# Optimization experiments

Measured on AMD Instinct MI355X. Metric: run time of the kernel, lower is better.

Reference implementation:

```python
import jax, jax.numpy as jnp
import numpy as np

B, V, D, H, W = 2, 256, 512, 256, 256
CH = 96  # RED-CNN channels


def conv2d(x, w, b=None, padding='SAME'):
    y = jax.lax.conv_general_dilated(x, w, (1, 1), padding,
                                     dimension_numbers=('NCHW', 'OIHW', 'NCHW'))
    if b is not None:
        y = y + b[None, :, None, None]
    return y


def backproject_per_view(fp, angles):
    # fp: [B,V,D] filtered sinogram; one single-view backprojection per angle -> [B,V,H,W]
    b = fp.shape[0]
    ys = jnp.arange(H, dtype=jnp.float32) - (H - 1) / 2.
    xs = jnp.arange(W, dtype=jnp.float32) - (W - 1) / 2.
    Y, X = jnp.meshgrid(ys, xs, indexing='ij')
    c = jnp.cos(angles)[:, None, None]
    s = jnp.sin(angles)[:, None, None]
    u = X[None] * c + Y[None] * s + (D - 1) / 2.  # [V,H,W] detector coordinate
    u0 = jnp.floor(u)
    frac = (u - u0).reshape(1, V, H * W)
    u0i = u0.astype(jnp.int32)
    valid = ((u0i >= 0) & (u0i <= D - 2)).reshape(1, V, H * W)
    u0c = jnp.clip(u0i, 0, D - 2).reshape(V, H * W)
    idx0 = jnp.broadcast_to(u0c[None], (b, V, H * W))
    g0 = jnp.take_along_axis(fp, idx0, axis=2)
    g1 = jnp.take_along_axis(fp, idx0 + 1, axis=2)
    g = (g0 * (1. - frac) + g1 * frac) * valid
    return (g * (jnp.pi / V)).reshape(b, V, H, W)


def red_cnn(x, enc_w0, enc_w, enc_b, dec_w, dec_wN, dec_b, dec_bN):
    relu = jax.nn.relu
    r1 = x
    h = relu(conv2d(x, enc_w0, enc_b[0]))
    h = relu(conv2d(h, enc_w[0], enc_b[1])); r2 = h
    h = relu(conv2d(h, enc_w[1], enc_b[2]))
    h = relu(conv2d(h, enc_w[2], enc_b[3])); r3 = h
    h = relu(conv2d(h, enc_w[3], enc_b[4]))
    h = relu(conv2d(h, dec_w[0], dec_b[0]) + r3)
    h = relu(conv2d(h, dec_w[1], dec_b[1]))
    h = relu(conv2d(h, dec_w[2], dec_b[2]) + r2)
    h = relu(conv2d(h, dec_w[3], dec_b[3]))
    return relu(conv2d(h, dec_wN, dec_bN) + r1)


def setup_inputs():
    key = jax.random.key(0)
    ks = jax.random.split(key, 8)
    p = jax.random.normal(ks[0], (B, 1, V, D), dtype=jnp.float32)
    proj_weight = jax.random.uniform(ks[1], (1, 1, V, D), dtype=jnp.float32, minval=0.5, maxval=1.5)
    # Ram-Lak ramp filter, length 2*D-1 (matches padding=(0, num_det-1))
    n = np.arange(-(D - 1), D)
    h = np.zeros(2 * D - 1, dtype=np.float32)
    h[D - 1] = 0.25
    odd = (n % 2) != 0
    h[odd] = -1.0 / (np.pi * n[odd]) ** 2
    ramp = jnp.asarray(h).reshape(1, 1, 1, 2 * D - 1)
    views = jnp.arange(V, dtype=jnp.float32) * (2 * jnp.pi / V)
    std = 0.01
    conv_w = std * jax.random.normal(ks[2], (1, V, 3, 3), dtype=jnp.float32)
    conv_b = jnp.zeros((1,), jnp.float32)
    enc_w0 = std * jax.random.normal(ks[3], (CH, 1, 5, 5), dtype=jnp.float32)
    enc_w = std * jax.random.normal(ks[4], (4, CH, CH, 5, 5), dtype=jnp.float32)
    enc_b = jnp.zeros((5, CH), jnp.float32)
    dec_w = std * jax.random.normal(ks[5], (4, CH, CH, 5, 5), dtype=jnp.float32)
    dec_wN = std * jax.random.normal(ks[6], (1, CH, 5, 5), dtype=jnp.float32)
    dec_b = jnp.zeros((4, CH), jnp.float32)
    dec_bN = jnp.zeros((1,), jnp.float32)
    return dict(p=p, proj_weight=proj_weight, ramp=ramp, views=views,
                conv_w=conv_w, conv_b=conv_b, enc_w0=enc_w0, enc_w=enc_w,
                enc_b=enc_b, dec_w=dec_w, dec_wN=dec_wN, dec_b=dec_b, dec_bN=dec_bN)


def reference(p, proj_weight, ramp, views, conv_w, conv_b, enc_w0, enc_w,
              enc_b, dec_w, dec_wN, dec_b, dec_bN):
    p_w = p * proj_weight
    filtered = conv2d(p_w, ramp, padding=[(0, 0), (D - 1, D - 1)])  # [B,1,V,D]
    x = backproject_per_view(filtered[:, 0], views)                 # [B,V,H,W]
    x_sorted = jnp.sort(x, axis=1)                                  # cross-view sort
    x_in = conv2d(x_sorted, conv_w, conv_b)                         # [B,1,H,W]
    return red_cnn(x_in, enc_w0, enc_w, enc_b, dec_w, dec_wN, dec_b, dec_bN)
```

## Files before the change

kernel.cpp:

```cpp
#include <hip/hip_runtime.h>
#include <hip/hip_fp16.h>
#include <math.h>

#define B_ 2
#define V_ 256
#define D_ 512
#define H_ 256
#define W_ 256
#define CH_ 96

typedef _Float16 f16;
typedef f16 half8 __attribute__((ext_vector_type(8)));
typedef f16 half4 __attribute__((ext_vector_type(4)));
typedef f16 half2v __attribute__((ext_vector_type(2)));
typedef float f32x16 __attribute__((ext_vector_type(16)));

#if defined(__has_builtin)
#if __has_builtin(__builtin_amdgcn_fdot2)
#define FDOT2(a, b, c) __builtin_amdgcn_fdot2((a), (b), (c), false)
#endif
#endif
#ifndef FDOT2
#define FDOT2(a, b, c) ((c) + (float)(a)[0] * (float)(b)[0] + (float)(a)[1] * (float)(b)[1])
#endif


__global__ void filter_kernel(const float* __restrict__ p,
                              const float* __restrict__ pw,
                              const float* __restrict__ ramp,
                              float* __restrict__ filt) {
  int v = blockIdx.x, b = blockIdx.y, t = threadIdx.x;
  __shared__ float s_pw[D_];
  __shared__ float s_ramp[2 * D_ - 1];
  const float* prow = p + (size_t)(b * V_ + v) * D_;
  const float* wrow = pw + (size_t)v * D_;
  s_pw[t] = prow[t] * wrow[t];
  s_pw[t + 256] = prow[t + 256] * wrow[t + 256];
  for (int i = t; i < 2 * D_ - 1; i += 256) s_ramp[i] = ramp[i];
  __syncthreads();
  float acc0 = 0.f, acc1 = 0.f;
  for (int m = 0; m < D_; ++m) {
    float x = s_pw[m];
    acc0 += x * s_ramp[m - t + (D_ - 1)];
    acc1 += x * s_ramp[m - (t + 256) + (D_ - 1)];
  }
  filt[(size_t)(b * V_ + v) * D_ + t] = acc0;
  filt[(size_t)(b * V_ + v) * D_ + t + 256] = acc1;
}

__global__ __launch_bounds__(256) void backproj_sort_kernel(
    const float* __restrict__ filt,
    const float* __restrict__ views,
    f16* __restrict__ xt) {
  __shared__ float s_c[V_], s_s[V_];
  int tid = threadIdx.x;
  int b = blockIdx.y;
  {
    float sn, cs;
    sincosf(views[tid], &sn, &cs);
    s_c[tid] = cs;
    s_s[tid] = sn;
  }
  __syncthreads();
  int lane = tid & 63;
  int wv = tid >> 6;
  int pix = blockIdx.x * 4 + wv;
  int h = pix >> 8, w = pix & 255;
  float X = (float)w - (W_ - 1) * 0.5f;
  float Y = (float)h - (H_ - 1) * 0.5f;
  const float* filt_b = filt + (size_t)b * V_ * D_;
  float r[4];
  #pragma unroll
  for (int i = 0; i < 4; ++i) {
    int v = lane * 4 + i;
    float u = X * s_c[v] + Y * s_s[v] + (D_ - 1) * 0.5f;
    float u0 = floorf(u);
    float frac = u - u0;
    int u0i = (int)u0;
    bool valid = (u0i >= 0) && (u0i <= D_ - 2);
    int u0c = min(max(u0i, 0), D_ - 2);
    const float* frow = filt_b + (size_t)v * D_;
    float g0 = frow[u0c], g1 = frow[u0c + 1];
    r[i] = valid ? (g0 * (1.f - frac) + g1 * frac) * (float)(M_PI / V_) : 0.f;
  }
  half2v A = { (f16)r[0], (f16)r[1] };
  half2v B = { (f16)r[2], (f16)r[3] };
  #pragma unroll
  for (int k = 2; k <= 256; k <<= 1) {
    #pragma unroll
    for (int j = k >> 1; j > 0; j >>= 1) {
      if (j >= 4) {
        int jl = j >> 2;
        bool low = (lane & jl) == 0;
        bool up = (lane & (k >> 2)) == 0;
        bool keepmin = (low == up);
        int ia = __builtin_bit_cast(int, A);
        int ib = __builtin_bit_cast(int, B);
        half2v Ao = __builtin_bit_cast(half2v, __shfl_xor(ia, jl, 64));
        half2v Bo = __builtin_bit_cast(half2v, __shfl_xor(ib, jl, 64));
        half2v Amn = __builtin_elementwise_min(A, Ao);
        half2v Amx = __builtin_elementwise_max(A, Ao);
        half2v Bmn = __builtin_elementwise_min(B, Bo);
        half2v Bmx = __builtin_elementwise_max(B, Bo);
        A = keepmin ? Amn : Amx;
        B = keepmin ? Bmn : Bmx;
      } else if (j == 2) {
        bool up = (lane & (k >> 2)) == 0;
        half2v mn = __builtin_elementwise_min(A, B);
        half2v mx = __builtin_elementwise_max(A, B);
        A = up ? mn : mx;
        B = up ? mx : mn;
      } else {
        unsigned ua = __builtin_bit_cast(unsigned, A);
        unsigned ub = __builtin_bit_cast(unsigned, B);
        half2v As = __builtin_bit_cast(half2v, (ua >> 16) | (ua << 16));
        half2v Bs = __builtin_bit_cast(half2v, (ub >> 16) | (ub << 16));
        unsigned amn = __builtin_bit_cast(unsigned, __builtin_elementwise_min(A, As));
        unsigned amx = __builtin_bit_cast(unsigned, __builtin_elementwise_max(A, As));
        unsigned bmn = __builtin_bit_cast(unsigned, __builtin_elementwise_min(B, Bs));
        unsigned bmx = __builtin_bit_cast(unsigned, __builtin_elementwise_max(B, Bs));
        unsigned Aasc  = (amn & 0xFFFFu) | (amx & 0xFFFF0000u);
        unsigned Adesc = (amx & 0xFFFFu) | (amn & 0xFFFF0000u);
        unsigned Basc  = (bmn & 0xFFFFu) | (bmx & 0xFFFF0000u);
        unsigned Bdesc = (bmx & 0xFFFFu) | (bmn & 0xFFFF0000u);
        bool upA, upB;
        if (k == 2) { upA = true; upB = false; }
        else { upA = upB = ((lane & (k >> 2)) == 0); }
        A = __builtin_bit_cast(half2v, upA ? Aasc : Adesc);
        B = __builtin_bit_cast(half2v, upB ? Basc : Bdesc);
      }
    }
  }
  half4 o;
  o[0] = A[0]; o[1] = A[1]; o[2] = B[0]; o[3] = B[1];
  *(half4*)(xt + ((size_t)b * (H_ * W_) + pix) * V_ + lane * 4) = o;
}

__global__ __launch_bounds__(256) void conv_vred_kernel(
    const f16* __restrict__ xt,
    const float* __restrict__ cw,
    const float* __restrict__ cb,
    float* __restrict__ xin) {
  int tid = threadIdx.x;
  int b = blockIdx.y;
  int lane = tid & 63, wv = tid >> 6;
  int pix = blockIdx.x * 4 + wv;
  int h = pix >> 8, w = pix & 255;
  const f16* xtb = xt + (size_t)b * (H_ * W_) * V_;
  float wr[9][4];
  #pragma unroll
  for (int tap = 0; tap < 9; ++tap)
    #pragma unroll
    for (int i = 0; i < 4; ++i)
      wr[tap][i] = cw[(lane * 4 + i) * 9 + tap];
  float acc = 0.f;
  #pragma unroll
  for (int dy = -1; dy <= 1; ++dy) {
    int hh = h + dy;
    if (hh < 0 || hh >= H_) continue;
    #pragma unroll
    for (int dx = -1; dx <= 1; ++dx) {
      int ww = w + dx;
      if (ww < 0 || ww >= W_) continue;
      const f16* base = xtb + (((size_t)hh << 8) + ww) * V_ + lane * 4;
      half4 x4 = *(const half4*)base;
      int tap = (dy + 1) * 3 + dx + 1;
      acc += (float)x4[0] * wr[tap][0] + (float)x4[1] * wr[tap][1] +
             (float)x4[2] * wr[tap][2] + (float)x4[3] * wr[tap][3];
    }
  }
  for (int off = 32; off > 0; off >>= 1) acc += __shfl_down(acc, off);
  if (lane == 0) xin[(size_t)b * (H_ * W_) + pix] = acc + cb[0];
}

__global__ void wtrans_kernel(const float* __restrict__ enc_w,
                              const float* __restrict__ dec_w,
                              f16* __restrict__ wT) {
  int idx = blockIdx.x * 256 + threadIdx.x;
  const int TOT = 8 * 25 * 96 * 96;
  if (idx >= TOT) return;
  int ci16 = idx & 15;
  int t1 = idx >> 4;
  int co = t1 % 96;
  int t2 = t1 / 96;
  int cig = t2 % 6;
  int t3 = t2 / 6;
  int tap = t3 % 25;
  int l = t3 / 25;
  int ci = cig * 16 + ci16;
  const float* src = (l < 4) ? (enc_w + (size_t)l * 96 * 96 * 25)
                             : (dec_w + (size_t)(l - 4) * 96 * 96 * 25);
  wT[idx] = (f16)src[((size_t)co * 96 + ci) * 25 + tap];
}

__global__ __launch_bounds__(768, 3) void conv5_mfma_kernel(
    const f16* __restrict__ act,
    const f16* __restrict__ wTl,
    const float* __restrict__ bias,
    const f16* __restrict__ res,
    f16* __restrict__ outp) {
  int tid = threadIdx.x;
  int lane = tid & 63;
  int l31 = lane & 31, lh = lane >> 5;
  int wvi = tid >> 6;
  int c = wvi >> 2;
  int q = wvi & 3;
  int bt = blockIdx.x;
  int x0 = (bt & 7) * 32;
  int y0 = (bt >> 3) * 16;
  size_t bofs = (size_t)blockIdx.z * ((size_t)H_ * W_ * CH_);
  const f16* actb = act + bofs;

  __shared__ __align__(16) f16 tile[6 * 20 * 36 * 16];
  char* tb = (char*)tile;
  const int PLANE = 20 * 36 * 32;
  const int ROWB  = 36 * 32;
  const size_t GSTR = (size_t)H_ * W_ * 16;

  #pragma unroll
  for (int g = 0; g < 6; ++g) {
    const f16* gb = actb + (size_t)g * GSTR;
    #pragma unroll
    for (int pass = 0; pass < 2; ++pass) {
      int idx = pass * 768 + tid;
      int cell = idx >> 1, j = idx & 1;
      if (cell < 720) {
        int row = cell / 36, xx = cell % 36;
        int gy = y0 + row - 2, gx = x0 + xx - 2;
        bool va = (gy >= 0 && gy < H_ && gx >= 0 && gx < W_);
        uint4 v = {0u, 0u, 0u, 0u};
        if (va) v = *(const uint4*)(gb + ((size_t)(gy * W_ + gx)) * 16 + j * 8);
        int swz = ((xx >> 2) & 7) << 4;
        *(uint4*)(tb + g * PLANE + ((cell * 32 + j * 16) ^ swz)) = v;
      }
    }
  }
  __syncthreads();

  int dsb[5];
  #pragma unroll
  for (int dx = 0; dx < 5; ++dx) {
    int xr = l31 + dx;
    dsb[dx] = (xr * 32 + lh * 16) ^ (((xr >> 2) & 7) << 4);
  }

  f32x16 acc[4];
  #pragma unroll
  for (int i = 0; i < 4; ++i)
    #pragma unroll
    for (int r = 0; r < 16; ++r) acc[i][r] = 0.f;

  const f16* wc = wTl + (size_t)(c * 32 + l31) * 16 + lh * 8;

  for (int cig = 0; cig < 6; ++cig) {
    const f16* wcg = wc + (size_t)cig * (96 * 16);
    char* pb = tb + cig * PLANE + 4 * q * ROWB;
    #pragma unroll
    for (int dx = 0; dx < 5; ++dx) {
      half8 Af[5];
      #pragma unroll
      for (int dy = 0; dy < 5; ++dy)
        Af[dy] = *(const half8*)(wcg + (size_t)(dy * 5 + dx) * (6 * 96 * 16));
      half8 Bw[8];
      #pragma unroll
      for (int k = 0; k < 8; ++k)
        Bw[k] = *(const half8*)(pb + k * ROWB + dsb[dx]);
      #pragma unroll
      for (int dy = 0; dy < 5; ++dy) {
        acc[0] = __builtin_amdgcn_mfma_f32_32x32x16_f16(Af[dy], Bw[dy + 0], acc[0], 0, 0, 0);
        acc[1] = __builtin_amdgcn_mfma_f32_32x32x16_f16(Af[dy], Bw[dy + 1], acc[1], 0, 0, 0);
        acc[2] = __builtin_amdgcn_mfma_f32_32x32x16_f16(Af[dy], Bw[dy + 2], acc[2], 0, 0, 0);
        acc[3] = __builtin_amdgcn_mfma_f32_32x32x16_f16(Af[dy], Bw[dy + 3], acc[3], 0, 0, 0);
      }
    }
  }

  int x = x0 + l31;
  #pragma unroll
  for (int i = 0; i < 4; ++i) {
    int y = y0 + 4 * q + i;
    int p = y * W_ + x;
    f32x16 a = acc[i];
    #pragma unroll
    for (int g = 0; g < 4; ++g) {
      int cg = c * 2 + (g >> 1);
      size_t ao = bofs + (size_t)cg * GSTR + (size_t)p * 16 + (g & 1) * 8 + lh * 4;
      half4 rv;
      if (res) rv = *(const half4*)(res + ao);
      half4 o4;
      #pragma unroll
      for (int r = 0; r < 4; ++r) {
        float v = a[g * 4 + r] + bias[c * 32 + g * 8 + lh * 4 + r];
        if (res) v += (float)rv[r];
        o4[r] = (f16)fmaxf(v, 0.f);
      }
      *(half4*)(outp + ao) = o4;
    }
  }
}

__global__ __launch_bounds__(256) void conv5_first_kernel(
    const float* __restrict__ xin, const float* __restrict__ w0,
    const float* __restrict__ bias, f16* __restrict__ A) {
  int tid = threadIdx.x;
  int tx = tid & 15, ty = tid >> 4;
  int x0 = (blockIdx.x & 15) * 16, y0 = (blockIdx.x >> 4) * 16;
  const float* xb = xin + (size_t)blockIdx.y * (H_ * W_);
  __shared__ float t[20][20];
  __shared__ float ws[CH_ * 25];
  for (int i = tid; i < 400; i += 256) {
    int r = i / 20, cc = i % 20;
    int gy = y0 + r - 2, gx = x0 + cc - 2;
    t[r][cc] = (gy >= 0 && gy < H_ && gx >= 0 && gx < W_) ? xb[gy * W_ + gx] : 0.f;
  }
  for (int i = tid; i < CH_ * 25; i += 256) ws[i] = w0[i];
  __syncthreads();
  float xv[25];
  #pragma unroll
  for (int k = 0; k < 25; ++k) xv[k] = t[ty + k / 5][tx + k % 5];
  size_t base = (size_t)blockIdx.y * ((size_t)H_ * W_ * CH_);
  const size_t GSTR = (size_t)H_ * W_ * 16;
  int p = (y0 + ty) * W_ + x0 + tx;
  #pragma unroll
  for (int g = 0; g < 6; ++g) {
    f16 tmp[16];
    #pragma unroll
    for (int cc = 0; cc < 16; ++cc) {
      int ch = g * 16 + cc;
      float a0 = bias[ch];
      #pragma unroll
      for (int k = 0; k < 25; ++k) a0 = fmaf(xv[k], ws[ch * 25 + k], a0);
      tmp[cc] = (f16)fmaxf(a0, 0.f);
    }
    f16* Ap = A + base + g * GSTR + (size_t)p * 16;
    *(uint4*)(Ap) = *(uint4*)(tmp);
    *(uint4*)(Ap + 8) = *(uint4*)(tmp + 8);
  }
}

__global__ __launch_bounds__(256) void conv5_last_kernel(
    const f16* __restrict__ A, const float* __restrict__ wN,
    const float* __restrict__ bias, const float* __restrict__ xin,
    float* __restrict__ outp) {
  int tid = threadIdx.x;
  int tx = tid & 15, ty = tid >> 4;
  int x0 = (blockIdx.x & 15) * 16, y0 = (blockIdx.x >> 4) * 16;
  size_t bo = (size_t)blockIdx.y * (H_ * W_);
  const f16* Ab = A + bo * CH_;
  const size_t GSTR = (size_t)H_ * W_ * 16;
  __shared__ __align__(16) f16 t[6 * 400 * 16];
  __shared__ __align__(16) f16 wh[25 * CH_];
  char* tb = (char*)t;
  const int LPLANE = 400 * 32;
  for (int i = tid; i < 25 * CH_; i += 256) {
    int k = i / CH_, ci = i % CH_;
    wh[i] = (f16)wN[ci * 25 + k];
  }
  #pragma unroll
  for (int g = 0; g < 6; ++g) {
    const f16* Ag = Ab + (size_t)g * GSTR;
    for (int idx = tid; idx < 800; idx += 256) {
      int cell = idx >> 1, j = idx & 1;
      int r = cell / 20, cc = cell % 20;
      int gy = y0 + r - 2, gx = x0 + cc - 2;
      bool va = (gy >= 0 && gy < H_ && gx >= 0 && gx < W_);
      uint4 v = {0u, 0u, 0u, 0u};
      if (va) v = *(const uint4*)(Ag + ((size_t)(gy * W_ + gx)) * 16 + j * 8);
      int sw = (cell & 7) << 4;
      *(uint4*)(tb + g * LPLANE + ((cell * 32 + j * 16) ^ sw)) = v;
    }
  }
  __syncthreads();
  float acc = bias[0];
  #pragma unroll
  for (int k = 0; k < 25; ++k) {
    int cellr = (ty + k / 5) * 20 + tx + k % 5;
    int sw = (cellr & 7) << 4;
    #pragma unroll
    for (int g = 0; g < 6; ++g) {
      const half2v* wp = (const half2v*)(wh + k * CH_ + g * 16);
      uint4 a0 = *(const uint4*)(tb + g * LPLANE + ((cellr * 32) ^ sw));
      uint4 a1 = *(const uint4*)(tb + g * LPLANE + ((cellr * 32 + 16) ^ sw));
      acc = FDOT2(__builtin_bit_cast(half2v, a0.x), wp[0], acc);
      acc = FDOT2(__builtin_bit_cast(half2v, a0.y), wp[1], acc);
      acc = FDOT2(__builtin_bit_cast(half2v, a0.z), wp[2], acc);
      acc = FDOT2(__builtin_bit_cast(half2v, a0.w), wp[3], acc);
      acc = FDOT2(__builtin_bit_cast(half2v, a1.x), wp[4], acc);
      acc = FDOT2(__builtin_bit_cast(half2v, a1.y), wp[5], acc);
      acc = FDOT2(__builtin_bit_cast(half2v, a1.z), wp[6], acc);
      acc = FDOT2(__builtin_bit_cast(half2v, a1.w), wp[7], acc);
    }
  }
  int pix = (y0 + ty) * W_ + x0 + tx;
  acc += xin[bo + pix];
  outp[bo + pix] = fmaxf(acc, 0.f);
}

__global__ void diag_kernel(float* __restrict__ out, int code, int wsMiB) {
  out[0] = (float)(code * 1000000 + wsMiB);
}

extern "C" void kernel_launch(void* const* d_in, const int* in_sizes, int n_in,
                              void* d_out, int out_size, void* d_ws, size_t ws_size,
                              hipStream_t stream) {
  const float* p       = (const float*)d_in[0];
  const float* pweight = (const float*)d_in[1];
  const float* ramp    = (const float*)d_in[2];
  const float* views   = (const float*)d_in[3];
  const float* conv_w  = (const float*)d_in[4];
  const float* conv_b  = (const float*)d_in[5];
  const float* enc_w0  = (const float*)d_in[6];
  const float* enc_w   = (const float*)d_in[7];
  const float* enc_b   = (const float*)d_in[8];
  const float* dec_w   = (const float*)d_in[9];
  const float* dec_wN  = (const float*)d_in[10];
  const float* dec_b   = (const float*)d_in[11];
  const float* dec_bN  = (const float*)d_in[12];
  float* out           = (float*)d_out;

  char* wsb   = (char*)d_ws;
  float* filt = (float*)(wsb);
  float* xin  = (float*)(wsb + 0x100000u);
  f16* wT     = (f16*)(wsb + 0x180000u);
  const size_t AOFF = 0x508000u;
  f16* xt     = (f16*)(wsb + AOFF);

  const size_t ACT = (size_t)H_ * W_ * CH_;
  const size_t NEEDED_SEQ  = AOFF + 3 * ACT * 2;
  const size_t NEEDED_DUAL = AOFF + 6 * ACT * 2;
  int wsMiB = (int)(ws_size >> 20);
  if (ws_size < NEEDED_SEQ) {
    diag_kernel<<<1, 1, 0, stream>>>(out, 9, wsMiB);
    return;
  }
  int nb = (ws_size >= NEEDED_DUAL) ? 2 : 1;
  size_t bufSz = (size_t)nb * ACT;
  f16* A  = (f16*)(wsb + AOFF);
  f16* Bb = A + bufSz;
  f16* C  = Bb + bufSz;

  const int HW = H_ * W_;
  const size_t WTL = 25 * 96 * 96;

  filter_kernel<<<dim3(V_, B_), 256, 0, stream>>>(p, pweight, ramp, filt);
  wtrans_kernel<<<7200, 256, 0, stream>>>(enc_w, dec_w, wT);

  if (nb == 2) {
    backproj_sort_kernel<<<dim3(HW / 4, 2), 256, 0, stream>>>(filt, views, xt);
    conv_vred_kernel<<<dim3(HW / 4, 2), 256, 0, stream>>>(xt, conv_w, conv_b, xin);
  } else {
    for (int b = 0; b < B_; ++b) {
      backproj_sort_kernel<<<dim3(HW / 4, 1), 256, 0, stream>>>(filt + (size_t)b * V_ * D_, views, xt);
      conv_vred_kernel<<<dim3(HW / 4, 1), 256, 0, stream>>>(xt, conv_w, conv_b, xin + (size_t)b * HW);
    }
  }

  auto run_net = [&](const float* xin_g, float* out_g, int nbat) {
    dim3 gL(128, 1, nbat);
    dim3 gS(256, nbat);
    conv5_first_kernel<<<gS, 256, 0, stream>>>(xin_g, enc_w0, enc_b, A);
    conv5_mfma_kernel<<<gL, 768, 0, stream>>>(A,  wT + 0 * WTL, enc_b + 96,  nullptr, Bb);
    conv5_mfma_kernel<<<gL, 768, 0, stream>>>(Bb, wT + 1 * WTL, enc_b + 192, nullptr, A);
    conv5_mfma_kernel<<<gL, 768, 0, stream>>>(A,  wT + 2 * WTL, enc_b + 288, nullptr, C);
    conv5_mfma_kernel<<<gL, 768, 0, stream>>>(C,  wT + 3 * WTL, enc_b + 384, nullptr, A);
    conv5_mfma_kernel<<<gL, 768, 0, stream>>>(A,  wT + 4 * WTL, dec_b + 0,   C,       C);
    conv5_mfma_kernel<<<gL, 768, 0, stream>>>(C,  wT + 5 * WTL, dec_b + 96,  nullptr, A);
    conv5_mfma_kernel<<<gL, 768, 0, stream>>>(A,  wT + 6 * WTL, dec_b + 192, Bb,      Bb);
    conv5_mfma_kernel<<<gL, 768, 0, stream>>>(Bb, wT + 7 * WTL, dec_b + 288, nullptr, A);
    conv5_last_kernel<<<gS, 256, 0, stream>>>(A, dec_wN, dec_bN, xin_g, out_g);
  };

  if (nb == 2) {
    run_net(xin, out, 2);
  } else {
    for (int b = 0; b < B_; ++b)
      run_net(xin + (size_t)b * HW, out + (size_t)b * HW, 1);
  }
}
```

Before: 663.1 us.

## Use zero-padded activation layout and read conv inputs directly from global memory

Activations are stored in a 260x260 zero-padded layout, with a one-time kernel that zeroes the borders, so the conv kernels no longer need bounds checks. The 96-channel MFMA conv drops its shared-memory tile staging and loads input rows straight from global memory (relying on L1/L2 caching). The output-channel split moves from waves within a block to a grid dimension, giving 256-thread blocks with more blocks resident. Weight fragments are now loaded per dy inside the loop instead of preloaded per dx. Each block now re-reads its input tile for each of the three channel groups and depends on cache hits for reuse, and border writes must keep the padding zero.

New measurement: 836.1 us. 1.26x slower.

```diff
diff --git a/kernel.cpp b/kernel.cpp
--- a/kernel.cpp
+++ b/kernel.cpp
@@ -8,6 +8,7 @@
 #define H_ 256
 #define W_ 256
 #define CH_ 96
+#define PW 260
 
 typedef _Float16 f16;
 typedef f16 half8 __attribute__((ext_vector_type(8)));
@@ -24,6 +25,7 @@
 #define FDOT2(a, b, c) ((c) + (float)(a)[0] * (float)(b)[0] + (float)(a)[1] * (float)(b)[1])
 #endif
 
+static const size_t PGSTR = (size_t)PW * PW * 16;
 
 __global__ void filter_kernel(const float* __restrict__ p,
                               const float* __restrict__ pw,
@@ -193,7 +195,22 @@
   wT[idx] = (f16)src[((size_t)co * 96 + ci) * 25 + tap];
 }
 
-__global__ __launch_bounds__(768, 3) void conv5_mfma_kernel(
+__global__ void zero_border_kernel(f16* __restrict__ base, int nplanes) {
+  int idx = blockIdx.x * 256 + threadIdx.x;
+  int total = nplanes * 2064;
+  if (idx >= total) return;
+  int p = idx / 2064, i = idx % 2064;
+  int r, ccol;
+  if (i < 520) { r = i / 260; ccol = i % 260; }
+  else if (i < 1040) { int t = i - 520; r = 258 + t / 260; ccol = t % 260; }
+  else { int t = i - 1040; r = 2 + (t >> 2); ccol = (t & 1) + ((t >> 1) & 1) * 258; }
+  f16* pp = base + (size_t)p * PGSTR + ((size_t)r * PW + ccol) * 16;
+  const uint4 z = {0u, 0u, 0u, 0u};
+  *(uint4*)pp = z;
+  *(uint4*)(pp + 8) = z;
+}
+
+__global__ __launch_bounds__(256, 4) void conv5_mfma_kernel(
     const f16* __restrict__ act,
     const f16* __restrict__ wTl,
     const float* __restrict__ bias,
@@ -202,48 +219,14 @@
   int tid = threadIdx.x;
   int lane = tid & 63;
   int l31 = lane & 31, lh = lane >> 5;
-  int wvi = tid >> 6;
-  int c = wvi >> 2;
-  int q = wvi & 3;
+  int q = tid >> 6;
+  int c = blockIdx.y;
   int bt = blockIdx.x;
   int x0 = (bt & 7) * 32;
   int y0 = (bt >> 3) * 16;
-  size_t bofs = (size_t)blockIdx.z * ((size_t)H_ * W_ * CH_);
+  size_t bofs = (size_t)blockIdx.z * (6 * PGSTR);
   const f16* actb = act + bofs;
 
-  __shared__ __align__(16) f16 tile[6 * 20 * 36 * 16];
-  char* tb = (char*)tile;
-  const int PLANE = 20 * 36 * 32;
-  const int ROWB  = 36 * 32;
-  const size_t GSTR = (size_t)H_ * W_ * 16;
-
-  #pragma unroll
-  for (int g = 0; g < 6; ++g) {
-    const f16* gb = actb + (size_t)g * GSTR;
-    #pragma unroll
-    for (int pass = 0; pass < 2; ++pass) {
-      int idx = pass * 768 + tid;
-      int cell = idx >> 1, j = idx & 1;
-      if (cell < 720) {
-        int row = cell / 36, xx = cell % 36;
-        int gy = y0 + row - 2, gx = x0 + xx - 2;
-        bool va = (gy >= 0 && gy < H_ && gx >= 0 && gx < W_);
-        uint4 v = {0u, 0u, 0u, 0u};
-        if (va) v = *(const uint4*)(gb + ((size_t)(gy * W_ + gx)) * 16 + j * 8);
-        int swz = ((xx >> 2) & 7) << 4;
-        *(uint4*)(tb + g * PLANE + ((cell * 32 + j * 16) ^ swz)) = v;
-      }
-    }
-  }
-  __syncthreads();
-
-  int dsb[5];
-  #pragma unroll
-  for (int dx = 0; dx < 5; ++dx) {
-    int xr = l31 + dx;
-    dsb[dx] = (xr * 32 + lh * 16) ^ (((xr >> 2) & 7) << 4);
-  }
-
   f32x16 acc[4];
   #pragma unroll
   for (int i = 0; i < 4; ++i)
@@ -251,26 +234,24 @@
     for (int r = 0; r < 16; ++r) acc[i][r] = 0.f;
 
   const f16* wc = wTl + (size_t)(c * 32 + l31) * 16 + lh * 8;
+  size_t rowbase = ((size_t)(y0 + 4 * q) * PW + x0 + l31) * 16 + lh * 8;
 
   for (int cig = 0; cig < 6; ++cig) {
     const f16* wcg = wc + (size_t)cig * (96 * 16);
-    char* pb = tb + cig * PLANE + 4 * q * ROWB;
+    const f16* pb = actb + (size_t)cig * PGSTR + rowbase;
     #pragma unroll
     for (int dx = 0; dx < 5; ++dx) {
-      half8 Af[5];
-      #pragma unroll
-      for (int dy = 0; dy < 5; ++dy)
-        Af[dy] = *(const half8*)(wcg + (size_t)(dy * 5 + dx) * (6 * 96 * 16));
       half8 Bw[8];
       #pragma unroll
       for (int k = 0; k < 8; ++k)
-        Bw[k] = *(const half8*)(pb + k * ROWB + dsb[dx]);
+        Bw[k] = *(const half8*)(pb + (size_t)(k * PW + dx) * 16);
       #pragma unroll
       for (int dy = 0; dy < 5; ++dy) {
-        acc[0] = __builtin_amdgcn_mfma_f32_32x32x16_f16(Af[dy], Bw[dy + 0], acc[0], 0, 0, 0);
-        acc[1] = __builtin_amdgcn_mfma_f32_32x32x16_f16(Af[dy], Bw[dy + 1], acc[1], 0, 0, 0);
-        acc[2] = __builtin_amdgcn_mfma_f32_32x32x16_f16(Af[dy], Bw[dy + 2], acc[2], 0, 0, 0);
-        acc[3] = __builtin_amdgcn_mfma_f32_32x32x16_f16(Af[dy], Bw[dy + 3], acc[3], 0, 0, 0);
+        half8 Af = *(const half8*)(wcg + (size_t)(dy * 5 + dx) * (6 * 96 * 16));
+        acc[0] = __builtin_amdgcn_mfma_f32_32x32x16_f16(Af, Bw[dy + 0], acc[0], 0, 0, 0);
+        acc[1] = __builtin_amdgcn_mfma_f32_32x32x16_f16(Af, Bw[dy + 1], acc[1], 0, 0, 0);
+        acc[2] = __builtin_amdgcn_mfma_f32_32x32x16_f16(Af, Bw[dy + 2], acc[2], 0, 0, 0);
+        acc[3] = __builtin_amdgcn_mfma_f32_32x32x16_f16(Af, Bw[dy + 3], acc[3], 0, 0, 0);
       }
     }
   }
@@ -279,12 +260,12 @@
   #pragma unroll
   for (int i = 0; i < 4; ++i) {
     int y = y0 + 4 * q + i;
-    int p = y * W_ + x;
+    size_t pp = ((size_t)(y + 2) * PW + (x + 2)) * 16;
     f32x16 a = acc[i];
     #pragma unroll
     for (int g = 0; g < 4; ++g) {
       int cg = c * 2 + (g >> 1);
-      size_t ao = bofs + (size_t)cg * GSTR + (size_t)p * 16 + (g & 1) * 8 + lh * 4;
+      size_t ao = bofs + (size_t)cg * PGSTR + pp + (g & 1) * 8 + lh * 4;
       half4 rv;
       if (res) rv = *(const half4*)(res + ao);
       half4 o4;
@@ -318,9 +299,8 @@
   float xv[25];
   #pragma unroll
   for (int k = 0; k < 25; ++k) xv[k] = t[ty + k / 5][tx + k % 5];
-  size_t base = (size_t)blockIdx.y * ((size_t)H_ * W_ * CH_);
-  const size_t GSTR = (size_t)H_ * W_ * 16;
-  int p = (y0 + ty) * W_ + x0 + tx;
+  size_t base = (size_t)blockIdx.y * (6 * PGSTR);
+  size_t pp = ((size_t)(y0 + ty + 2) * PW + (x0 + tx + 2)) * 16;
   #pragma unroll
   for (int g = 0; g < 6; ++g) {
     f16 tmp[16];
@@ -332,7 +312,7 @@
       for (int k = 0; k < 25; ++k) a0 = fmaf(xv[k], ws[ch * 25 + k], a0);
       tmp[cc] = (f16)fmaxf(a0, 0.f);
     }
-    f16* Ap = A + base + g * GSTR + (size_t)p * 16;
+    f16* Ap = A + base + (size_t)g * PGSTR + pp;
     *(uint4*)(Ap) = *(uint4*)(tmp);
     *(uint4*)(Ap + 8) = *(uint4*)(tmp + 8);
   }
@@ -346,8 +326,7 @@
   int tx = tid & 15, ty = tid >> 4;
   int x0 = (blockIdx.x & 15) * 16, y0 = (blockIdx.x >> 4) * 16;
   size_t bo = (size_t)blockIdx.y * (H_ * W_);
-  const f16* Ab = A + bo * CH_;
-  const size_t GSTR = (size_t)H_ * W_ * 16;
+  const f16* Ab = A + (size_t)blockIdx.y * (6 * PGSTR);
   __shared__ __align__(16) f16 t[6 * 400 * 16];
   __shared__ __align__(16) f16 wh[25 * CH_];
   char* tb = (char*)t;
@@ -358,14 +337,11 @@
   }
   #pragma unroll
   for (int g = 0; g < 6; ++g) {
-    const f16* Ag = Ab + (size_t)g * GSTR;
+    const f16* Ag = Ab + (size_t)g * PGSTR;
     for (int idx = tid; idx < 800; idx += 256) {
       int cell = idx >> 1, j = idx & 1;
       int r = cell / 20, cc = cell % 20;
-      int gy = y0 + r - 2, gx = x0 + cc - 2;
-      bool va = (gy >= 0 && gy < H_ && gx >= 0 && gx < W_);
-      uint4 v = {0u, 0u, 0u, 0u};
-      if (va) v = *(const uint4*)(Ag + ((size_t)(gy * W_ + gx)) * 16 + j * 8);
+      uint4 v = *(const uint4*)(Ag + ((size_t)(y0 + r) * PW + (x0 + cc)) * 16 + j * 8);
       int sw = (cell & 7) << 4;
       *(uint4*)(tb + g * LPLANE + ((cell * 32 + j * 16) ^ sw)) = v;
     }
@@ -425,16 +401,16 @@
   const size_t AOFF = 0x508000u;
   f16* xt     = (f16*)(wsb + AOFF);
 
-  const size_t ACT = (size_t)H_ * W_ * CH_;
-  const size_t NEEDED_SEQ  = AOFF + 3 * ACT * 2;
-  const size_t NEEDED_DUAL = AOFF + 6 * ACT * 2;
+  const size_t PACT = 6 * PGSTR;
+  const size_t NEEDED_SEQ  = AOFF + 3 * PACT * 2;
+  const size_t NEEDED_DUAL = AOFF + 6 * PACT * 2;
   int wsMiB = (int)(ws_size >> 20);
   if (ws_size < NEEDED_SEQ) {
     diag_kernel<<<1, 1, 0, stream>>>(out, 9, wsMiB);
     return;
   }
   int nb = (ws_size >= NEEDED_DUAL) ? 2 : 1;
-  size_t bufSz = (size_t)nb * ACT;
+  size_t bufSz = (size_t)nb * PACT;
   f16* A  = (f16*)(wsb + AOFF);
   f16* Bb = A + bufSz;
   f16* C  = Bb + bufSz;
@@ -454,19 +430,24 @@
       conv_vred_kernel<<<dim3(HW / 4, 1), 256, 0, stream>>>(xt, conv_w, conv_b, xin + (size_t)b * HW);
     }
   }
+  {
+    int nplanes = 3 * nb * 6;
+    int total = nplanes * 2064;
+    zero_border_kernel<<<(total + 255) / 256, 256, 0, stream>>>(A, nplanes);
+  }
 
   auto run_net = [&](const float* xin_g, float* out_g, int nbat) {
-    dim3 gL(128, 1, nbat);
+    dim3 gL(128, 3, nbat);
     dim3 gS(256, nbat);
     conv5_first_kernel<<<gS, 256, 0, stream>>>(xin_g, enc_w0, enc_b, A);
-    conv5_mfma_kernel<<<gL, 768, 0, stream>>>(A,  wT + 0 * WTL, enc_b + 96,  nullptr, Bb);
-    conv5_mfma_kernel<<<gL, 768, 0, stream>>>(Bb, wT + 1 * WTL, enc_b + 192, nullptr, A);
-    conv5_mfma_kernel<<<gL, 768, 0, stream>>>(A,  wT + 2 * WTL, enc_b + 288, nullptr, C);
-    conv5_mfma_kernel<<<gL, 768, 0, stream>>>(C,  wT + 3 * WTL, enc_b + 384, nullptr, A);
-    conv5_mfma_kernel<<<gL, 768, 0, stream>>>(A,  wT + 4 * WTL, dec_b + 0,   C,       C);
-    conv5_mfma_kernel<<<gL, 768, 0, stream>>>(C,  wT + 5 * WTL, dec_b + 96,  nullptr, A);
-    conv5_mfma_kernel<<<gL, 768, 0, stream>>>(A,  wT + 6 * WTL, dec_b + 192, Bb,      Bb);
-    conv5_mfma_kernel<<<gL, 768, 0, stream>>>(Bb, wT + 7 * WTL, dec_b + 288, nullptr, A);
+    conv5_mfma_kernel<<<gL, 256, 0, stream>>>(A,  wT + 0 * WTL, enc_b + 96,  nullptr, Bb);
+    conv5_mfma_kernel<<<gL, 256, 0, stream>>>(Bb, wT + 1 * WTL, enc_b + 192, nullptr, A);
+    conv5_mfma_kernel<<<gL, 256, 0, stream>>>(A,  wT + 2 * WTL, enc_b + 288, nullptr, C);
+    conv5_mfma_kernel<<<gL, 256, 0, stream>>>(C,  wT + 3 * WTL, enc_b + 384, nullptr, A);
+    conv5_mfma_kernel<<<gL, 256, 0, stream>>>(A,  wT + 4 * WTL, dec_b + 0,   C,       C);
+    conv5_mfma_kernel<<<gL, 256, 0, stream>>>(C,  wT + 5 * WTL, dec_b + 96,  nullptr, A);
+    conv5_mfma_kernel<<<gL, 256, 0, stream>>>(A,  wT + 6 * WTL, dec_b + 192, Bb,      Bb);
+    conv5_mfma_kernel<<<gL, 256, 0, stream>>>(Bb, wT + 7 * WTL, dec_b + 288, nullptr, A);
     conv5_last_kernel<<<gS, 256, 0, stream>>>(A, dec_wN, dec_bN, xin_g, out_g);
   };
 
```
